# Kernel tuning notes

Hardware: AMD Instinct MI355X
Metric: run time of the kernel (lower is better)

## Reference

```python
import jax, jax.numpy as jnp
import numpy as np

B, S, H, NH = 2, 2048, 1024, 16
DK = H // NH

def setup_inputs() -> dict:
    key = jax.random.key(0)
    ks = jax.random.split(key, 12)
    scale = 0.02
    return {
        "Q": jax.random.normal(ks[0], (B, S, H), jnp.float32),
        "K": jax.random.normal(ks[1], (B, S, H), jnp.float32),
        "V": jax.random.normal(ks[2], (B, S, H), jnp.float32),
        "attn_mask": jax.random.randint(ks[3], (B, S, S), 0, 2).astype(bool),
        "Wq": jax.random.normal(ks[4], (H, H), jnp.float32) * scale,
        "bq": jnp.zeros((H,), jnp.float32),
        "Wk": jax.random.normal(ks[5], (H, H), jnp.float32) * scale,
        "bk": jnp.zeros((H,), jnp.float32),
        "Wv": jax.random.normal(ks[6], (H, H), jnp.float32) * scale,
        "bv": jnp.zeros((H,), jnp.float32),
        "Wo": jax.random.normal(ks[7], (H, H), jnp.float32) * scale,
        "bo": jnp.zeros((H,), jnp.float32),
    }

def reference(Q, K, V, attn_mask, Wq, bq, Wk, bk, Wv, bv, Wo, bo):
    b = Q.shape[0]
    # linear projections (torch nn.Linear: x @ W.T + b), split heads -> [b, nh, s, dk]
    def proj(x, W, bias):
        return (x @ W.T + bias).reshape(b, -1, NH, DK).transpose(0, 2, 1, 3)
    q = proj(Q, Wq, bq)
    k = proj(K, Wk, bk)
    v = proj(V, Wv, bv)
    scores = jnp.einsum("bhqd,bhkd->bhqk", q, k) / jnp.sqrt(jnp.float32(DK))
    scores = jnp.where(attn_mask[:, None, :, :], jnp.float32(-1e9), scores)
    attn = jax.nn.softmax(scores, axis=-1)  # dropout prob = 0.0 (identity)
    ctx = jnp.einsum("bhqk,bhkd->bhqd", attn, v)
    ctx = ctx.transpose(0, 2, 1, 3).reshape(b, -1, NH * DK)
    return ctx @ Wo.T + bo
```

## Files before the change

kernel.cpp:

```cpp
#include <hip/hip_runtime.h>
#include <hip/hip_bf16.h>

typedef short s16x8 __attribute__((ext_vector_type(8)));
typedef float f32x4 __attribute__((ext_vector_type(4)));
typedef unsigned short u16;
typedef unsigned int u32;
typedef unsigned long long u64;

#define DEVI __device__ __forceinline__

#if __has_builtin(__builtin_amdgcn_exp2f)
#define EXP2F(x) __builtin_amdgcn_exp2f(x)
#else
#define EXP2F(x) exp2f(x)
#endif

#define QSCALE 0.1803368801111204f

DEVI float bf2f(u16 u){ union { u32 i; float f; } v; v.i = ((u32)u) << 16; return v.f; }
DEVI u16 f2bf(float f){ union { float f; u32 i; } v; v.f = f; u32 u = v.i;
                        return (u16)((u + 0x7fffu + ((u >> 16) & 1u)) >> 16); }

DEVI u32 pkbf2(float a, float b){
  union { __hip_bfloat162 h; u32 u; } v;
  v.h = __float22bfloat162_rn(make_float2(a, b));
  return v.u;
}
DEVI u64 pk4(float a, float b, float c, float d){
  return (u64)pkbf2(a, b) | ((u64)pkbf2(c, d) << 32);
}

DEVI f32x4 mfma_bf16(s16x8 a, s16x8 b, f32x4 c){
  return __builtin_amdgcn_mfma_f32_16x16x32_bf16(a, b, c, 0, 0, 0);
}

#define GLDS(gp, lp) __builtin_amdgcn_global_load_lds( \
    (const __attribute__((address_space(1))) void*)(gp), \
    (__attribute__((address_space(3))) void*)(lp), 16, 0, 0)

DEVI float4 cvt8f32(const float* p){
  float4 x = *(const float4*)p;
  float4 y = *(const float4*)(p + 4);
  union { u32 t[4]; float4 f4; } u;
  u.t[0] = pkbf2(x.x, x.y); u.t[1] = pkbf2(x.z, x.w);
  u.t[2] = pkbf2(y.x, y.y); u.t[3] = pkbf2(y.z, y.w);
  return u.f4;
}

DEVI bool detect_f32(const u16* probe){
  __shared__ int dsum[4];
  const int tid = threadIdx.x;
  int bad = 0;
#pragma unroll
  for (int i = 0; i < 16; ++i){
    u16 u = probe[tid * 16 + i];
    int e = (u >> 7) & 0xFF;
    bad += (e != 0 && (e < 100 || e > 150)) ? 1 : 0;
  }
#pragma unroll
  for (int o = 1; o < 64; o <<= 1) bad += __shfl_xor(bad, o);
  if ((tid & 63) == 0) dsum[tid >> 6] = bad;
  __syncthreads();
  bool r = (dsum[0] + dsum[1] + dsum[2] + dsum[3]) > 64;
  __syncthreads();
  return r;
}

struct PrepArgs { const void* src[7]; void* dst[7]; u32 coff[8]; };

__global__ __launch_bounds__(256) void prep_mask(PrepArgs a, const u16* probe,
                                                 const int* __restrict__ mask,
                                                 u64* __restrict__ bits,
                                                 int do_mask, int do_conv){
  if (blockIdx.x < 1024){
    if (!do_mask) return;
    const int lane = threadIdx.x & 63, wid = threadIdx.x >> 6;
    const int row = blockIdx.x * 4 + wid;
    const int* mrow = mask + (size_t)row * 2048;
    for (int c = 0; c < 32; ++c){
      int v = mrow[c * 64 + lane];
      u64 w = __ballot(v == 0);
      if (lane == 0) bits[(size_t)row * 32 + c] = w;
    }
  } else {
    if (!do_conv) return;
    const bool f32 = detect_f32(probe);
    if (!f32) return;
    const u32 total = a.coff[7];
    for (u32 c = (blockIdx.x - 1024) * 256 + threadIdx.x; c < total; c += 2048 * 256){
      int s = 0;
#pragma unroll
      for (int i = 1; i < 7; ++i) s += (c >= a.coff[i]) ? 1 : 0;
      u32 lc = c - a.coff[s];
      ((float4*)a.dst[s])[lc] = cvt8f32((const float*)a.src[s] + (size_t)lc * 8);
    }
  }
}

struct ProjP {
  const void* X[3];   const u16* Xc[3];
  const void* W[3];   const u16* Wc[3];
  const void* bias[3];
  u16* out[3];
  const u16* probe;
  int conv_ok;
};

__global__ __launch_bounds__(256) void proj_gemm(ProjP p){
  __shared__ u16 As[128 * 64];
  __shared__ u16 Bs[128 * 64];
  const int z = blockIdx.z;
  const bool in32 = detect_f32(p.probe);
  const bool f32st = in32 && !p.conv_ok;
  const u16* Ab = (in32 && p.conv_ok) ? p.Xc[z] : (const u16*)p.X[z];
  const u16* Wb = (in32 && p.conv_ok) ? p.Wc[z] : (const u16*)p.W[z];
  const float* Af = (const float*)p.X[z];
  const float* Wf = (const float*)p.W[z];
  const int tid = threadIdx.x;
  const int lane = tid & 63, wid = tid >> 6;
  const int quad = lane >> 4, l15 = lane & 15;
  const int m0 = blockIdx.y * 128, n0 = blockIdx.x * 128;
  const int wm = (wid >> 1) * 64, wn = (wid & 1) * 64;
  const int K = 1024;

  f32x4 acc[4][4];
  const f32x4 z4 = {0.f, 0.f, 0.f, 0.f};
  for (int i = 0; i < 4; ++i) for (int j = 0; j < 4; ++j) acc[i][j] = z4;

  for (int ko = 0; ko < 16; ++ko){
    const int kk = ko * 64;
    if (f32st){
#pragma unroll
      for (int i = 0; i < 4; ++i){
        int g = tid * 4 + i;
        int row = g >> 3, c = g & 7;
        *(float4*)(As + row * 64 + ((c ^ (row & 7)) * 8)) =
            cvt8f32(Af + (size_t)(m0 + row) * K + kk + c * 8);
        *(float4*)(Bs + row * 64 + ((c ^ (row & 7)) * 8)) =
            cvt8f32(Wf + (size_t)(n0 + row) * K + kk + c * 8);
      }
    } else {
#pragma unroll
      for (int i = 0; i < 4; ++i){
        int ci = (wid * 4 + i) * 64 + lane;
        int row = ci >> 3, gcc = (ci & 7) ^ (row & 7);
        GLDS(Ab + (size_t)(m0 + row) * K + kk + gcc * 8, As + (size_t)(wid * 4 + i) * 512);
        GLDS(Wb + (size_t)(n0 + row) * K + kk + gcc * 8, Bs + (size_t)(wid * 4 + i) * 512);
      }
    }
    __syncthreads();
#pragma unroll
    for (int ks = 0; ks < 2; ++ks){
      s16x8 af[4], bfr[4];
#pragma unroll
      for (int mt = 0; mt < 4; ++mt){
        int row = wm + mt * 16 + l15;
        af[mt] = *(const s16x8*)(As + row * 64 + (((ks * 4 + quad) ^ (row & 7)) * 8));
      }
#pragma unroll
      for (int nt = 0; nt < 4; ++nt){
        int row = wn + nt * 16 + l15;
        bfr[nt] = *(const s16x8*)(Bs + row * 64 + (((ks * 4 + quad) ^ (row & 7)) * 8));
      }
#pragma unroll
      for (int mt = 0; mt < 4; ++mt)
#pragma unroll
        for (int nt = 0; nt < 4; ++nt)
          acc[mt][nt] = mfma_bf16(af[mt], bfr[nt], acc[mt][nt]);
    }
    __syncthreads();
  }

  u16* outp = p.out[z];
#pragma unroll
  for (int nt = 0; nt < 4; ++nt){
    int col = n0 + wn + nt * 16 + l15;
    float bv = in32 ? ((const float*)p.bias[z])[col] : bf2f(((const u16*)p.bias[z])[col]);
#pragma unroll
    for (int mt = 0; mt < 4; ++mt){
      if (z == 2){
        int srow = m0 + wm + mt * 16 + quad * 4;
        int b = srow >> 11, s = srow & 2047, hh = col >> 6, d = col & 63;
        size_t idx = (((size_t)(b * 16 + hh)) * 64 + d) * 2048 + s;
        *(u64*)(outp + idx) = pk4(acc[mt][nt][0] + bv, acc[mt][nt][1] + bv,
                                  acc[mt][nt][2] + bv, acc[mt][nt][3] + bv);
      } else {
#pragma unroll
        for (int r = 0; r < 4; ++r){
          int row = m0 + wm + mt * 16 + quad * 4 + r;
          float v = acc[mt][nt][r] + bv;
          if (z == 0) v *= QSCALE;
          int b = row >> 11, s = row & 2047, hh = col >> 6, d = col & 63;
          outp[(((size_t)(b * 16 + hh)) * 2048 + s) * 64 + d] = f2bf(v);
        }
      }
    }
  }
}

__global__ __launch_bounds__(256) void gemm_out(const u16* __restrict__ A,
                                                const void* __restrict__ Wv,
                                                const u16* __restrict__ Wbf,
                                                const void* __restrict__ biasv,
                                                void* __restrict__ outv,
                                                const u16* __restrict__ probe,
                                                int conv_ok){
  __shared__ u16 As[64 * 64];
  __shared__ u16 Bs[64 * 64];
  const bool in32 = detect_f32(probe);
  const bool f32st = in32 && !conv_ok;
  const u16* Wb = (in32 && conv_ok) ? Wbf : (const u16*)Wv;
  const float* Wf = (const float*)Wv;
  const int tid = threadIdx.x;
  const int lane = tid & 63, wid = tid >> 6;
  const int quad = lane >> 4, l15 = lane & 15;
  const int m0 = blockIdx.y * 64, n0 = blockIdx.x * 64;
  const int wm = (wid >> 1) * 32, wn = (wid & 1) * 32;
  const int K = 1024;

  f32x4 acc[2][2];
  const f32x4 z4 = {0.f, 0.f, 0.f, 0.f};
  for (int i = 0; i < 2; ++i) for (int j = 0; j < 2; ++j) acc[i][j] = z4;

  for (int ko = 0; ko < 16; ++ko){
    const int kk = ko * 64;
#pragma unroll
    for (int i = 0; i < 2; ++i){
      int ci = (wid * 2 + i) * 64 + lane;
      int row = ci >> 3, gcc = (ci & 7) ^ (row & 7);
      GLDS(A + (size_t)(m0 + row) * K + kk + gcc * 8, As + (size_t)(wid * 2 + i) * 512);
    }
    if (f32st){
#pragma unroll
      for (int i = 0; i < 2; ++i){
        int g = tid * 2 + i;
        int row = g >> 3, c = g & 7;
        *(float4*)(Bs + row * 64 + ((c ^ (row & 7)) * 8)) =
            cvt8f32(Wf + (size_t)(n0 + row) * K + kk + c * 8);
      }
    } else {
#pragma unroll
      for (int i = 0; i < 2; ++i){
        int ci = (wid * 2 + i) * 64 + lane;
        int row = ci >> 3, gcc = (ci & 7) ^ (row & 7);
        GLDS(Wb + (size_t)(n0 + row) * K + kk + gcc * 8, Bs + (size_t)(wid * 2 + i) * 512);
      }
    }
    __syncthreads();
#pragma unroll
    for (int ks = 0; ks < 2; ++ks){
      s16x8 af[2], bfr[2];
#pragma unroll
      for (int mt = 0; mt < 2; ++mt){
        int row = wm + mt * 16 + l15;
        af[mt] = *(const s16x8*)(As + row * 64 + (((ks * 4 + quad) ^ (row & 7)) * 8));
      }
#pragma unroll
      for (int nt = 0; nt < 2; ++nt){
        int row = wn + nt * 16 + l15;
        bfr[nt] = *(const s16x8*)(Bs + row * 64 + (((ks * 4 + quad) ^ (row & 7)) * 8));
      }
#pragma unroll
      for (int mt = 0; mt < 2; ++mt)
#pragma unroll
        for (int nt = 0; nt < 2; ++nt)
          acc[mt][nt] = mfma_bf16(af[mt], bfr[nt], acc[mt][nt]);
    }
    __syncthreads();
  }

#pragma unroll
  for (int nt = 0; nt < 2; ++nt){
    int col = n0 + wn + nt * 16 + l15;
    float bv = in32 ? ((const float*)biasv)[col] : bf2f(((const u16*)biasv)[col]);
#pragma unroll
    for (int mt = 0; mt < 2; ++mt)
#pragma unroll
      for (int r = 0; r < 4; ++r){
        int row = m0 + wm + mt * 16 + quad * 4 + r;
        float v = acc[mt][nt][r] + bv;
        size_t idx = (size_t)row * 1024 + col;
        if (in32) ((float*)outv)[idx] = v;
        else      ((u16*)outv)[idx]   = f2bf(v);
      }
  }
}

__global__ __launch_bounds__(256, 2) void attn2(const u16* __restrict__ qws,
                                                const u16* __restrict__ kws,
                                                const u16* __restrict__ vtws,
                                                const u64* __restrict__ mbits,
                                                const int* __restrict__ rawmask,
                                                int use_raw,
                                                u16* __restrict__ ctxws){
  __shared__ u16 Ks[2][64 * 64];
  __shared__ u16 Vt[2][64 * 64];
  __shared__ u16 Ps[4][32 * 64];
  const int tid = threadIdx.x;
  const int lane = tid & 63, wid = tid >> 6;
  const int quad = lane >> 4, l15 = lane & 15;
  const int h = blockIdx.x, qt = blockIdx.y, b = blockIdx.z;
  const int q0 = qt * 128;
  const size_t bh = (size_t)(b * 16 + h) * (2048 * 64);
  int qrow[2];
  qrow[0] = q0 + wid * 32 + l15;
  qrow[1] = qrow[0] + 16;

  s16x8 qf[2][2];
#pragma unroll
  for (int rg = 0; rg < 2; ++rg)
#pragma unroll
    for (int ks = 0; ks < 2; ++ks)
      qf[rg][ks] = *(const s16x8*)(qws + bh + (size_t)qrow[rg] * 64 + ks * 32 + quad * 8);

  const f32x4 z4 = {0.f, 0.f, 0.f, 0.f};
  f32x4 ctx[2][4];
#pragma unroll
  for (int rg = 0; rg < 2; ++rg)
    for (int dt = 0; dt < 4; ++dt) ctx[rg][dt] = z4;
  f32x4 lacc[2] = {z4, z4};
  const short ONE = (short)0x3F80;
  const s16x8 ones8 = {ONE, ONE, ONE, ONE, ONE, ONE, ONE, ONE};

  u16* pp = &Ps[wid][0];
  u32 pw[2][4];
#pragma unroll
  for (int rg = 0; rg < 2; ++rg)
#pragma unroll
    for (int ntk = 0; ntk < 4; ++ntk)
      pw[rg][ntk] = (rg * 16 + l15) * 64 +
                    (((u32)(ntk * 2 + (quad >> 1)) ^ (u32)(l15 & 7)) * 8) + (quad & 1) * 4;

  const u64* mrow0 = mbits + ((size_t)(b * 2048 + qrow[0])) * 32;
  const u64* mrow1 = mbits + ((size_t)(b * 2048 + qrow[1])) * 32;

  const int sci = wid * 2;
  int srow0, sgc0, srow1, sgc1;
  {
    int ci0 = sci * 64 + lane;
    srow0 = ci0 >> 3; sgc0 = (ci0 & 7) ^ (srow0 & 7);
    int ci1 = (sci + 1) * 64 + lane;
    srow1 = ci1 >> 3; sgc1 = (ci1 & 7) ^ (srow1 & 7);
  }
  const u16* kp0 = kws + bh + (size_t)srow0 * 64 + sgc0 * 8;
  const u16* kp1 = kws + bh + (size_t)srow1 * 64 + sgc1 * 8;
  const u16* vp0 = vtws + bh + (size_t)srow0 * 2048 + sgc0 * 8;
  const u16* vp1 = vtws + bh + (size_t)srow1 * 2048 + sgc1 * 8;

  GLDS(kp0, &Ks[0][0] + (size_t)sci * 512);
  GLDS(vp0, &Vt[0][0] + (size_t)sci * 512);
  GLDS(kp1, &Ks[0][0] + (size_t)(sci + 1) * 512);
  GLDS(vp1, &Vt[0][0] + (size_t)(sci + 1) * 512);
  kp0 += 4096; kp1 += 4096; vp0 += 64; vp1 += 64;

  for (int kt = 0; kt < 32; kt += 2){
#pragma unroll
    for (int hb = 0; hb < 2; ++hb){
      const int t = kt + hb;
      const u16* kb = &Ks[hb][0];
      const u16* vb = &Vt[hb][0];
      __syncthreads();

      u64 mw0 = 0, mw1 = 0;
      if (!use_raw){ mw0 = mrow0[t]; mw1 = mrow1[t]; }

      if (t < 31){
        u16* kd = &Ks[hb ^ 1][0];
        u16* vd = &Vt[hb ^ 1][0];
        GLDS(kp0, kd + (size_t)sci * 512);
        GLDS(vp0, vd + (size_t)sci * 512);
        GLDS(kp1, kd + (size_t)(sci + 1) * 512);
        GLDS(vp1, vd + (size_t)(sci + 1) * 512);
        kp0 += 4096; kp1 += 4096; vp0 += 64; vp1 += 64;
      }

      f32x4 s[2][4];
#pragma unroll
      for (int rg = 0; rg < 2; ++rg)
#pragma unroll
        for (int ntk = 0; ntk < 4; ++ntk) s[rg][ntk] = z4;
#pragma unroll
      for (int ks = 0; ks < 2; ++ks)
#pragma unroll
        for (int ntk = 0; ntk < 4; ++ntk){
          int row = ntk * 16 + l15;
          s16x8 kf = *(const s16x8*)(kb + row * 64 + (((ks * 4 + quad) ^ (row & 7)) * 8));
          s[0][ntk] = mfma_bf16(kf, qf[0][ks], s[0][ntk]);
          s[1][ntk] = mfma_bf16(kf, qf[1][ks], s[1][ntk]);
        }

      if (!use_raw){
#pragma unroll
        for (int rg = 0; rg < 2; ++rg){
          u64 w = (rg ? mw1 : mw0) >> (quad * 4);
          u32 wlo = (u32)w, whi = (u32)(w >> 32);
#pragma unroll
          for (int ntk = 0; ntk < 4; ++ntk){
            u32 half32 = (ntk < 2) ? wlo : whi;
#pragma unroll
            for (int r = 0; r < 4; ++r){
              u32 keep = half32 & (1u << ((ntk & 1) * 16 + r));
              float sv = keep ? s[rg][ntk][r] : -1.0e9f;
              s[rg][ntk][r] = EXP2F(sv);
            }
          }
        }
      } else {
        const int k0 = t * 64;
#pragma unroll
        for (int rg = 0; rg < 2; ++rg)
#pragma unroll
          for (int ntk = 0; ntk < 4; ++ntk)
#pragma unroll
            for (int r = 0; r < 4; ++r){
              int key = k0 + ntk * 16 + quad * 4 + r;
              int mv = rawmask[((size_t)(b * 2048 + qrow[rg])) * 2048 + key];
              s[rg][ntk][r] = EXP2F(mv ? -1.0e9f : s[rg][ntk][r]);
            }
      }

#pragma unroll
      for (int rg = 0; rg < 2; ++rg)
#pragma unroll
        for (int ntk = 0; ntk < 4; ++ntk){
          uint2 tt;
          tt.x = pkbf2(s[rg][ntk][0], s[rg][ntk][1]);
          tt.y = pkbf2(s[rg][ntk][2], s[rg][ntk][3]);
          *(uint2*)(pp + pw[rg][ntk]) = tt;
        }
      s16x8 pf[2][2];
#pragma unroll
      for (int rg = 0; rg < 2; ++rg)
#pragma unroll
        for (int ks = 0; ks < 2; ++ks)
          pf[rg][ks] = *(const s16x8*)(pp + (rg * 16 + l15) * 64 +
                                       (((ks * 4 + quad) ^ (l15 & 7)) * 8));

#pragma unroll
      for (int ks = 0; ks < 2; ++ks){
#pragma unroll
        for (int dt = 0; dt < 4; ++dt){
          int row = dt * 16 + l15;
          s16x8 vf = *(const s16x8*)(vb + row * 64 + (((ks * 4 + quad) ^ (row & 7)) * 8));
          ctx[0][dt] = mfma_bf16(vf, pf[0][ks], ctx[0][dt]);
          ctx[1][dt] = mfma_bf16(vf, pf[1][ks], ctx[1][dt]);
        }
        lacc[0] = mfma_bf16(ones8, pf[0][ks], lacc[0]);
        lacc[1] = mfma_bf16(ones8, pf[1][ks], lacc[1]);
      }
    }
  }

#pragma unroll
  for (int rg = 0; rg < 2; ++rg){
    float inv = 1.0f / fmaxf(lacc[rg][0], 1e-30f);
#pragma unroll
    for (int dt = 0; dt < 4; ++dt){
      int d0 = dt * 16 + quad * 4;
      u64 w = pk4(ctx[rg][dt][0] * inv, ctx[rg][dt][1] * inv,
                  ctx[rg][dt][2] * inv, ctx[rg][dt][3] * inv);
      *(u64*)(ctxws + ((size_t)(b * 2048 + qrow[rg])) * 1024 + h * 64 + d0) = w;
    }
  }
}

extern "C" void kernel_launch(void* const* d_in, const int* in_sizes, int n_in,
                              void* d_out, int out_size, void* d_ws, size_t ws_size,
                              hipStream_t stream){
  const void* Q    = d_in[0];
  const void* Kin  = d_in[1];
  const void* Vin  = d_in[2];
  const int* mask  = (const int*)d_in[3];
  const void* Wq = d_in[4];  const void* bq = d_in[5];
  const void* Wk = d_in[6];  const void* bk = d_in[7];
  const void* Wv = d_in[8];  const void* bv = d_in[9];
  const void* Wo = d_in[10]; const void* bo = d_in[11];

  char* ws = (char*)d_ws;
  const size_t MB = 1u << 20;
  const bool small_ws = ws_size < 33 * MB;
  const bool big_ws   = ws_size >= 66 * MB;
  u64* mbits = (u64*)ws;
  const size_t base = small_ws ? 0 : MB;
  u16* qws  = (u16*)(ws + base);
  u16* kws  = (u16*)(ws + base + 8 * MB);
  u16* vtws = (u16*)(ws + base + 16 * MB);
  u16* cws  = (u16*)(ws + base + 24 * MB);
  u16* Qc  = (u16*)(ws + 33 * MB);
  u16* Kc  = (u16*)(ws + 41 * MB);
  u16* Vc  = (u16*)(ws + 49 * MB);
  u16* Wqc = (u16*)(ws + 57 * MB);
  u16* Wkc = (u16*)(ws + 59 * MB);
  u16* Wvc = (u16*)(ws + 61 * MB);
  u16* Woc = (u16*)(ws + 63 * MB);
  const u16* probe = (const u16*)Q;

  PrepArgs pa;
  pa.src[0] = Q;  pa.src[1] = Kin; pa.src[2] = Vin;
  pa.src[3] = Wq; pa.src[4] = Wk;  pa.src[5] = Wv; pa.src[6] = Wo;
  pa.dst[0] = Qc;  pa.dst[1] = Kc;  pa.dst[2] = Vc;
  pa.dst[3] = Wqc; pa.dst[4] = Wkc; pa.dst[5] = Wvc; pa.dst[6] = Woc;
  const u32 cq = 4194304 / 8, cw = 1048576 / 8;
  pa.coff[0] = 0;
  pa.coff[1] = cq;          pa.coff[2] = 2 * cq;      pa.coff[3] = 3 * cq;
  pa.coff[4] = 3 * cq + cw; pa.coff[5] = 3 * cq + 2 * cw;
  pa.coff[6] = 3 * cq + 3 * cw; pa.coff[7] = 3 * cq + 4 * cw;
  prep_mask<<<dim3(3072), 256, 0, stream>>>(pa, probe, mask, mbits,
                                            small_ws ? 0 : 1, big_ws ? 1 : 0);

  ProjP pp;
  pp.X[0] = Q;  pp.X[1] = Kin; pp.X[2] = Vin;
  pp.Xc[0] = Qc; pp.Xc[1] = Kc; pp.Xc[2] = Vc;
  pp.W[0] = Wq; pp.W[1] = Wk; pp.W[2] = Wv;
  pp.Wc[0] = Wqc; pp.Wc[1] = Wkc; pp.Wc[2] = Wvc;
  pp.bias[0] = bq; pp.bias[1] = bk; pp.bias[2] = bv;
  pp.out[0] = qws; pp.out[1] = kws; pp.out[2] = vtws;
  pp.probe = probe;
  pp.conv_ok = big_ws ? 1 : 0;
  proj_gemm<<<dim3(8, 32, 3), 256, 0, stream>>>(pp);

  attn2<<<dim3(16, 16, 2), 256, 0, stream>>>(qws, kws, vtws, mbits, mask,
                                             small_ws ? 1 : 0, cws);

  gemm_out<<<dim3(16, 64), 256, 0, stream>>>(cws, Wo, Woc, bo, d_out, probe,
                                             big_ws ? 1 : 0);
}
```

Measured before the change: 274.3 us.

## Double-buffer shared-memory tiles in projection and output GEMMs

Both projection and output GEMM kernels switch to two shared-memory buffers, issuing the global-to-LDS loads for the next K tile before computing the current one, with one barrier per step instead of two. The projection GEMM narrows the K tile from 64 to 32 (same total LDS) and uses a 4-way XOR swizzle. The aim is to hide global load latency behind MFMA work. The cost is more loop iterations and barriers in proj_gemm and doubled LDS use in gemm_out, which could lower occupancy.

```diff
diff --git a/kernel.cpp b/kernel.cpp
--- a/kernel.cpp
+++ b/kernel.cpp
@@ -107,8 +107,8 @@
 };
 
 __global__ __launch_bounds__(256) void proj_gemm(ProjP p){
-  __shared__ u16 As[128 * 64];
-  __shared__ u16 Bs[128 * 64];
+  __shared__ u16 As[2][128 * 32];
+  __shared__ u16 Bs[2][128 * 32];
   const int z = blockIdx.z;
   const bool in32 = detect_f32(p.probe);
   const bool f32st = in32 && !p.conv_ok;
@@ -127,40 +127,61 @@
   const f32x4 z4 = {0.f, 0.f, 0.f, 0.f};
   for (int i = 0; i < 4; ++i) for (int j = 0; j < 4; ++j) acc[i][j] = z4;
 
-  for (int ko = 0; ko < 16; ++ko){
-    const int kk = ko * 64;
-    if (f32st){
-#pragma unroll
-      for (int i = 0; i < 4; ++i){
-        int g = tid * 4 + i;
-        int row = g >> 3, c = g & 7;
-        *(float4*)(As + row * 64 + ((c ^ (row & 7)) * 8)) =
-            cvt8f32(Af + (size_t)(m0 + row) * K + kk + c * 8);
-        *(float4*)(Bs + row * 64 + ((c ^ (row & 7)) * 8)) =
-            cvt8f32(Wf + (size_t)(n0 + row) * K + kk + c * 8);
-      }
-    } else {
-#pragma unroll
-      for (int i = 0; i < 4; ++i){
-        int ci = (wid * 4 + i) * 64 + lane;
-        int row = ci >> 3, gcc = (ci & 7) ^ (row & 7);
-        GLDS(Ab + (size_t)(m0 + row) * K + kk + gcc * 8, As + (size_t)(wid * 4 + i) * 512);
-        GLDS(Wb + (size_t)(n0 + row) * K + kk + gcc * 8, Bs + (size_t)(wid * 4 + i) * 512);
-      }
-    }
-    __syncthreads();
-#pragma unroll
-    for (int ks = 0; ks < 2; ++ks){
+  const int ci0 = wid * 2, ci1 = wid * 2 + 1;
+  const int ar0 = ci0 * 16 + (lane >> 2), ag0 = (lane & 3) ^ (ar0 & 3);
+  const int ar1 = ci1 * 16 + (lane >> 2), ag1 = (lane & 3) ^ (ar1 & 3);
+  const u16* pa0 = Ab + (size_t)(m0 + ar0) * K + ag0 * 8;
+  const u16* pa1 = Ab + (size_t)(m0 + ar1) * K + ag1 * 8;
+  const u16* pb0 = Wb + (size_t)(n0 + ar0) * K + ag0 * 8;
+  const u16* pb1 = Wb + (size_t)(n0 + ar1) * K + ag1 * 8;
+
+  const int fg0 = tid * 2, fg1 = tid * 2 + 1;
+  const int fr0 = fg0 >> 2, fc0 = fg0 & 3, fp0 = fr0 * 32 + ((fc0 ^ (fr0 & 3)) * 8);
+  const int fr1 = fg1 >> 2, fc1 = fg1 & 3, fp1 = fr1 * 32 + ((fc1 ^ (fr1 & 3)) * 8);
+
+  if (f32st){
+    *(float4*)(&As[0][0] + fp0) = cvt8f32(Af + (size_t)(m0 + fr0) * K + fc0 * 8);
+    *(float4*)(&As[0][0] + fp1) = cvt8f32(Af + (size_t)(m0 + fr1) * K + fc1 * 8);
+    *(float4*)(&Bs[0][0] + fp0) = cvt8f32(Wf + (size_t)(n0 + fr0) * K + fc0 * 8);
+    *(float4*)(&Bs[0][0] + fp1) = cvt8f32(Wf + (size_t)(n0 + fr1) * K + fc1 * 8);
+  } else {
+    GLDS(pa0, &As[0][0] + ci0 * 512);
+    GLDS(pa1, &As[0][0] + ci1 * 512);
+    GLDS(pb0, &Bs[0][0] + ci0 * 512);
+    GLDS(pb1, &Bs[0][0] + ci1 * 512);
+    pa0 += 32; pa1 += 32; pb0 += 32; pb1 += 32;
+  }
+
+  for (int ko = 0; ko < 32; ko += 2){
+#pragma unroll
+    for (int hb = 0; hb < 2; ++hb){
+      const int t = ko + hb;
+      __syncthreads();
+      if (t < 31){
+        if (f32st){
+          const int kk = (t + 1) * 32;
+          *(float4*)(&As[hb ^ 1][0] + fp0) = cvt8f32(Af + (size_t)(m0 + fr0) * K + kk + fc0 * 8);
+          *(float4*)(&As[hb ^ 1][0] + fp1) = cvt8f32(Af + (size_t)(m0 + fr1) * K + kk + fc1 * 8);
+          *(float4*)(&Bs[hb ^ 1][0] + fp0) = cvt8f32(Wf + (size_t)(n0 + fr0) * K + kk + fc0 * 8);
+          *(float4*)(&Bs[hb ^ 1][0] + fp1) = cvt8f32(Wf + (size_t)(n0 + fr1) * K + kk + fc1 * 8);
+        } else {
+          GLDS(pa0, &As[hb ^ 1][0] + ci0 * 512);
+          GLDS(pa1, &As[hb ^ 1][0] + ci1 * 512);
+          GLDS(pb0, &Bs[hb ^ 1][0] + ci0 * 512);
+          GLDS(pb1, &Bs[hb ^ 1][0] + ci1 * 512);
+          pa0 += 32; pa1 += 32; pb0 += 32; pb1 += 32;
+        }
+      }
       s16x8 af[4], bfr[4];
 #pragma unroll
       for (int mt = 0; mt < 4; ++mt){
         int row = wm + mt * 16 + l15;
-        af[mt] = *(const s16x8*)(As + row * 64 + (((ks * 4 + quad) ^ (row & 7)) * 8));
+        af[mt] = *(const s16x8*)(&As[hb][0] + row * 32 + ((quad ^ (row & 3)) * 8));
       }
 #pragma unroll
       for (int nt = 0; nt < 4; ++nt){
         int row = wn + nt * 16 + l15;
-        bfr[nt] = *(const s16x8*)(Bs + row * 64 + (((ks * 4 + quad) ^ (row & 7)) * 8));
+        bfr[nt] = *(const s16x8*)(&Bs[hb][0] + row * 32 + ((quad ^ (row & 3)) * 8));
       }
 #pragma unroll
       for (int mt = 0; mt < 4; ++mt)
@@ -168,7 +189,6 @@
         for (int nt = 0; nt < 4; ++nt)
           acc[mt][nt] = mfma_bf16(af[mt], bfr[nt], acc[mt][nt]);
     }
-    __syncthreads();
   }
 
   u16* outp = p.out[z];
@@ -205,8 +225,8 @@
                                                 void* __restrict__ outv,
                                                 const u16* __restrict__ probe,
                                                 int conv_ok){
-  __shared__ u16 As[64 * 64];
-  __shared__ u16 Bs[64 * 64];
+  __shared__ u16 As[2][64 * 64];
+  __shared__ u16 Bs[2][64 * 64];
   const bool in32 = detect_f32(probe);
   const bool f32st = in32 && !conv_ok;
   const u16* Wb = (in32 && conv_ok) ? Wbf : (const u16*)Wv;
@@ -222,51 +242,70 @@
   const f32x4 z4 = {0.f, 0.f, 0.f, 0.f};
   for (int i = 0; i < 2; ++i) for (int j = 0; j < 2; ++j) acc[i][j] = z4;
 
-  for (int ko = 0; ko < 16; ++ko){
-    const int kk = ko * 64;
-#pragma unroll
-    for (int i = 0; i < 2; ++i){
-      int ci = (wid * 2 + i) * 64 + lane;
-      int row = ci >> 3, gcc = (ci & 7) ^ (row & 7);
-      GLDS(A + (size_t)(m0 + row) * K + kk + gcc * 8, As + (size_t)(wid * 2 + i) * 512);
-    }
-    if (f32st){
-#pragma unroll
-      for (int i = 0; i < 2; ++i){
-        int g = tid * 2 + i;
-        int row = g >> 3, c = g & 7;
-        *(float4*)(Bs + row * 64 + ((c ^ (row & 7)) * 8)) =
-            cvt8f32(Wf + (size_t)(n0 + row) * K + kk + c * 8);
-      }
-    } else {
-#pragma unroll
-      for (int i = 0; i < 2; ++i){
-        int ci = (wid * 2 + i) * 64 + lane;
-        int row = ci >> 3, gcc = (ci & 7) ^ (row & 7);
-        GLDS(Wb + (size_t)(n0 + row) * K + kk + gcc * 8, Bs + (size_t)(wid * 2 + i) * 512);
-      }
-    }
-    __syncthreads();
-#pragma unroll
-    for (int ks = 0; ks < 2; ++ks){
-      s16x8 af[2], bfr[2];
-#pragma unroll
-      for (int mt = 0; mt < 2; ++mt){
-        int row = wm + mt * 16 + l15;
-        af[mt] = *(const s16x8*)(As + row * 64 + (((ks * 4 + quad) ^ (row & 7)) * 8));
-      }
-#pragma unroll
-      for (int nt = 0; nt < 2; ++nt){
-        int row = wn + nt * 16 + l15;
-        bfr[nt] = *(const s16x8*)(Bs + row * 64 + (((ks * 4 + quad) ^ (row & 7)) * 8));
-      }
-#pragma unroll
-      for (int mt = 0; mt < 2; ++mt)
-#pragma unroll
-        for (int nt = 0; nt < 2; ++nt)
-          acc[mt][nt] = mfma_bf16(af[mt], bfr[nt], acc[mt][nt]);
-    }
-    __syncthreads();
+  const int ci0 = wid * 2, ci1 = wid * 2 + 1;
+  const int e0 = ci0 * 64 + lane, e1 = ci1 * 64 + lane;
+  const int ar0 = e0 >> 3, ag0 = (e0 & 7) ^ (ar0 & 7);
+  const int ar1 = e1 >> 3, ag1 = (e1 & 7) ^ (ar1 & 7);
+  const u16* pa0 = A + (size_t)(m0 + ar0) * K + ag0 * 8;
+  const u16* pa1 = A + (size_t)(m0 + ar1) * K + ag1 * 8;
+  const u16* pb0 = Wb + (size_t)(n0 + ar0) * K + ag0 * 8;
+  const u16* pb1 = Wb + (size_t)(n0 + ar1) * K + ag1 * 8;
+
+  const int fg0 = tid * 2, fg1 = tid * 2 + 1;
+  const int fr0 = fg0 >> 3, fc0 = fg0 & 7, fp0 = fr0 * 64 + ((fc0 ^ (fr0 & 7)) * 8);
+  const int fr1 = fg1 >> 3, fc1 = fg1 & 7, fp1 = fr1 * 64 + ((fc1 ^ (fr1 & 7)) * 8);
+
+  GLDS(pa0, &As[0][0] + ci0 * 512);
+  GLDS(pa1, &As[0][0] + ci1 * 512);
+  if (f32st){
+    *(float4*)(&Bs[0][0] + fp0) = cvt8f32(Wf + (size_t)(n0 + fr0) * K + fc0 * 8);
+    *(float4*)(&Bs[0][0] + fp1) = cvt8f32(Wf + (size_t)(n0 + fr1) * K + fc1 * 8);
+  } else {
+    GLDS(pb0, &Bs[0][0] + ci0 * 512);
+    GLDS(pb1, &Bs[0][0] + ci1 * 512);
+    pb0 += 64; pb1 += 64;
+  }
+  pa0 += 64; pa1 += 64;
+
+  for (int ko = 0; ko < 16; ko += 2){
+#pragma unroll
+    for (int hb = 0; hb < 2; ++hb){
+      const int t = ko + hb;
+      __syncthreads();
+      if (t < 15){
+        GLDS(pa0, &As[hb ^ 1][0] + ci0 * 512);
+        GLDS(pa1, &As[hb ^ 1][0] + ci1 * 512);
+        pa0 += 64; pa1 += 64;
+        if (f32st){
+          const int kk = (t + 1) * 64;
+          *(float4*)(&Bs[hb ^ 1][0] + fp0) = cvt8f32(Wf + (size_t)(n0 + fr0) * K + kk + fc0 * 8);
+          *(float4*)(&Bs[hb ^ 1][0] + fp1) = cvt8f32(Wf + (size_t)(n0 + fr1) * K + kk + fc1 * 8);
+        } else {
+          GLDS(pb0, &Bs[hb ^ 1][0] + ci0 * 512);
+          GLDS(pb1, &Bs[hb ^ 1][0] + ci1 * 512);
+          pb0 += 64; pb1 += 64;
+        }
+      }
+#pragma unroll
+      for (int ks = 0; ks < 2; ++ks){
+        s16x8 af[2], bfr[2];
+#pragma unroll
+        for (int mt = 0; mt < 2; ++mt){
+          int row = wm + mt * 16 + l15;
+          af[mt] = *(const s16x8*)(&As[hb][0] + row * 64 + (((ks * 4 + quad) ^ (row & 7)) * 8));
+        }
+#pragma unroll
+        for (int nt = 0; nt < 2; ++nt){
+          int row = wn + nt * 16 + l15;
+          bfr[nt] = *(const s16x8*)(&Bs[hb][0] + row * 64 + (((ks * 4 + quad) ^ (row & 7)) * 8));
+        }
+#pragma unroll
+        for (int mt = 0; mt < 2; ++mt)
+#pragma unroll
+          for (int nt = 0; nt < 2; ++nt)
+            acc[mt][nt] = mfma_bf16(af[mt], bfr[nt], acc[mt][nt]);
+      }
+    }
   }
 
 #pragma unroll
```

Result: no change. 279.5 us (+1.9%).

## Split attention key range across two blocks and merge with a reduce kernel

Applied to the files above, without the earlier changes.

Splits the attention key loop into two halves handled by separate blocks, doubling the grid from 512 to 1024 blocks so the GPU's compute units are better filled. Each half writes a normalized bf16 context plus its row sum, and a new reduce kernel combines them weighted by the sums. The per-wave P staging buffer is halved by processing the two row groups one at a time, reducing LDS use. The cost is an extra kernel launch, extra global traffic for the partial contexts, and an added bf16 rounding step on the partials. Because the softmax uses no running max, the two halves merge by simple weighted sums.

```diff
diff --git a/kernel.cpp b/kernel.cpp
--- a/kernel.cpp
+++ b/kernel.cpp
@@ -292,14 +292,20 @@
                                                 const u64* __restrict__ mbits,
                                                 const int* __restrict__ rawmask,
                                                 int use_raw,
-                                                u16* __restrict__ ctxws){
+                                                u16* __restrict__ ctxws,
+                                                u16* __restrict__ ctx0,
+                                                u16* __restrict__ ctx1,
+                                                float* __restrict__ lsum,
+                                                int nsplit){
   __shared__ u16 Ks[2][64 * 64];
   __shared__ u16 Vt[2][64 * 64];
-  __shared__ u16 Ps[4][32 * 64];
+  __shared__ u16 Ps[4][16 * 64];
   const int tid = threadIdx.x;
   const int lane = tid & 63, wid = tid >> 6;
   const int quad = lane >> 4, l15 = lane & 15;
-  const int h = blockIdx.x, qt = blockIdx.y, b = blockIdx.z;
+  const int h = blockIdx.x, qt = blockIdx.y;
+  const int b = blockIdx.z / nsplit, half = blockIdx.z % nsplit;
+  const int nt = 32 / nsplit, t0 = half * nt;
   const int q0 = qt * 128;
   const size_t bh = (size_t)(b * 16 + h) * (2048 * 64);
   int qrow[2];
@@ -323,13 +329,10 @@
   const s16x8 ones8 = {ONE, ONE, ONE, ONE, ONE, ONE, ONE, ONE};
 
   u16* pp = &Ps[wid][0];
-  u32 pw[2][4];
-#pragma unroll
-  for (int rg = 0; rg < 2; ++rg)
-#pragma unroll
-    for (int ntk = 0; ntk < 4; ++ntk)
-      pw[rg][ntk] = (rg * 16 + l15) * 64 +
-                    (((u32)(ntk * 2 + (quad >> 1)) ^ (u32)(l15 & 7)) * 8) + (quad & 1) * 4;
+  u32 pw[4];
+#pragma unroll
+  for (int ntk = 0; ntk < 4; ++ntk)
+    pw[ntk] = l15 * 64 + (((u32)(ntk * 2 + (quad >> 1)) ^ (u32)(l15 & 7)) * 8) + (quad & 1) * 4;
 
   const u64* mrow0 = mbits + ((size_t)(b * 2048 + qrow[0])) * 32;
   const u64* mrow1 = mbits + ((size_t)(b * 2048 + qrow[1])) * 32;
@@ -342,10 +345,10 @@
     int ci1 = (sci + 1) * 64 + lane;
     srow1 = ci1 >> 3; sgc1 = (ci1 & 7) ^ (srow1 & 7);
   }
-  const u16* kp0 = kws + bh + (size_t)srow0 * 64 + sgc0 * 8;
-  const u16* kp1 = kws + bh + (size_t)srow1 * 64 + sgc1 * 8;
-  const u16* vp0 = vtws + bh + (size_t)srow0 * 2048 + sgc0 * 8;
-  const u16* vp1 = vtws + bh + (size_t)srow1 * 2048 + sgc1 * 8;
+  const u16* kp0 = kws + bh + (size_t)(t0 * 64 + srow0) * 64 + sgc0 * 8;
+  const u16* kp1 = kws + bh + (size_t)(t0 * 64 + srow1) * 64 + sgc1 * 8;
+  const u16* vp0 = vtws + bh + (size_t)srow0 * 2048 + t0 * 64 + sgc0 * 8;
+  const u16* vp1 = vtws + bh + (size_t)srow1 * 2048 + t0 * 64 + sgc1 * 8;
 
   GLDS(kp0, &Ks[0][0] + (size_t)sci * 512);
   GLDS(vp0, &Vt[0][0] + (size_t)sci * 512);
@@ -353,10 +356,10 @@
   GLDS(vp1, &Vt[0][0] + (size_t)(sci + 1) * 512);
   kp0 += 4096; kp1 += 4096; vp0 += 64; vp1 += 64;
 
-  for (int kt = 0; kt < 32; kt += 2){
+  for (int li = 0; li < nt; li += 2){
 #pragma unroll
     for (int hb = 0; hb < 2; ++hb){
-      const int t = kt + hb;
+      const int t = t0 + li + hb;
       const u16* kb = &Ks[hb][0];
       const u16* vb = &Vt[hb][0];
       __syncthreads();
@@ -364,7 +367,7 @@
       u64 mw0 = 0, mw1 = 0;
       if (!use_raw){ mw0 = mrow0[t]; mw1 = mrow1[t]; }
 
-      if (t < 31){
+      if (li + hb < nt - 1){
         u16* kd = &Ks[hb ^ 1][0];
         u16* vd = &Vt[hb ^ 1][0];
         GLDS(kp0, kd + (size_t)sci * 512);
@@ -419,22 +422,20 @@
             }
       }
 
-#pragma unroll
-      for (int rg = 0; rg < 2; ++rg)
+      s16x8 pf[2][2];
+#pragma unroll
+      for (int rg = 0; rg < 2; ++rg){
 #pragma unroll
         for (int ntk = 0; ntk < 4; ++ntk){
           uint2 tt;
           tt.x = pkbf2(s[rg][ntk][0], s[rg][ntk][1]);
           tt.y = pkbf2(s[rg][ntk][2], s[rg][ntk][3]);
-          *(uint2*)(pp + pw[rg][ntk]) = tt;
+          *(uint2*)(pp + pw[ntk]) = tt;
         }
-      s16x8 pf[2][2];
-#pragma unroll
-      for (int rg = 0; rg < 2; ++rg)
 #pragma unroll
         for (int ks = 0; ks < 2; ++ks)
-          pf[rg][ks] = *(const s16x8*)(pp + (rg * 16 + l15) * 64 +
-                                       (((ks * 4 + quad) ^ (l15 & 7)) * 8));
+          pf[rg][ks] = *(const s16x8*)(pp + l15 * 64 + (((ks * 4 + quad) ^ (l15 & 7)) * 8));
+      }
 
 #pragma unroll
       for (int ks = 0; ks < 2; ++ks){
@@ -451,6 +452,7 @@
     }
   }
 
+  u16* outp = (nsplit == 1) ? ctxws : (half == 0 ? ctx0 : ctx1);
 #pragma unroll
   for (int rg = 0; rg < 2; ++rg){
     float inv = 1.0f / fmaxf(lacc[rg][0], 1e-30f);
@@ -459,9 +461,40 @@
       int d0 = dt * 16 + quad * 4;
       u64 w = pk4(ctx[rg][dt][0] * inv, ctx[rg][dt][1] * inv,
                   ctx[rg][dt][2] * inv, ctx[rg][dt][3] * inv);
-      *(u64*)(ctxws + ((size_t)(b * 2048 + qrow[rg])) * 1024 + h * 64 + d0) = w;
-    }
-  }
+      *(u64*)(outp + ((size_t)(b * 2048 + qrow[rg])) * 1024 + h * 64 + d0) = w;
+    }
+  }
+  if (nsplit > 1 && quad == 0){
+    lsum[(size_t)half * 131072u + (size_t)(b * 2048 + qrow[0]) * 16 + h] = lacc[0][0];
+    lsum[(size_t)half * 131072u + (size_t)(b * 2048 + qrow[1]) * 16 + h] = lacc[1][0];
+  }
+}
+
+__global__ __launch_bounds__(256) void attn_reduce(const u16* __restrict__ c0p,
+                                                   const u16* __restrict__ c1p,
+                                                   const float* __restrict__ lsum,
+                                                   u16* __restrict__ out){
+  const u32 i = blockIdx.x * 256 + threadIdx.x;
+  const size_t o = (size_t)i * 8;
+  const u32 row = i >> 7;
+  const u32 h = (i >> 3) & 15;
+  float l0 = lsum[(size_t)row * 16 + h];
+  float l1 = lsum[131072u + (size_t)row * 16 + h];
+  float inv = 1.f / fmaxf(l0 + l1, 1e-30f);
+  float w0 = l0 * inv, w1 = l1 * inv;
+  uint4 a = *(const uint4*)(c0p + o);
+  uint4 b = *(const uint4*)(c1p + o);
+  u32 av[4] = {a.x, a.y, a.z, a.w};
+  u32 bv[4] = {b.x, b.y, b.z, b.w};
+  u32 rv[4];
+#pragma unroll
+  for (int j = 0; j < 4; ++j){
+    float x0 = bf2f((u16)av[j]) * w0 + bf2f((u16)bv[j]) * w1;
+    float x1 = bf2f((u16)(av[j] >> 16)) * w0 + bf2f((u16)(bv[j] >> 16)) * w1;
+    rv[j] = pkbf2(x0, x1);
+  }
+  uint4 r; r.x = rv[0]; r.y = rv[1]; r.z = rv[2]; r.w = rv[3];
+  *(uint4*)(out + o) = r;
 }
 
 extern "C" void kernel_launch(void* const* d_in, const int* in_sizes, int n_in,
@@ -480,6 +513,7 @@
   const size_t MB = 1u << 20;
   const bool small_ws = ws_size < 33 * MB;
   const bool big_ws   = ws_size >= 66 * MB;
+  const bool split    = ws_size >= 50 * MB;
   u64* mbits = (u64*)ws;
   const size_t base = small_ws ? 0 : MB;
   u16* qws  = (u16*)(ws + base);
@@ -493,6 +527,9 @@
   u16* Wkc = (u16*)(ws + 59 * MB);
   u16* Wvc = (u16*)(ws + 61 * MB);
   u16* Woc = (u16*)(ws + 63 * MB);
+  u16* ctx0   = (u16*)(ws + 33 * MB);
+  u16* ctx1   = (u16*)(ws + 41 * MB);
+  float* lsva = (float*)(ws + 49 * MB);
   const u16* probe = (const u16*)Q;
 
   PrepArgs pa;
@@ -519,8 +556,11 @@
   pp.conv_ok = big_ws ? 1 : 0;
   proj_gemm<<<dim3(8, 32, 3), 256, 0, stream>>>(pp);
 
-  attn2<<<dim3(16, 16, 2), 256, 0, stream>>>(qws, kws, vtws, mbits, mask,
-                                             small_ws ? 1 : 0, cws);
+  attn2<<<dim3(16, 16, split ? 4 : 2), 256, 0, stream>>>(
+      qws, kws, vtws, mbits, mask, small_ws ? 1 : 0, cws,
+      ctx0, ctx1, lsva, split ? 2 : 1);
+  if (split)
+    attn_reduce<<<dim3(2048), 256, 0, stream>>>(ctx0, ctx1, lsva, cws);
 
   gemm_out<<<dim3(16, 64), 256, 0, stream>>>(cws, Wo, Woc, bo, d_out, probe,
                                              big_ws ? 1 : 0);
```

Result: slower. 284.5 us (+3.7%).
